# Performance work log

Measured on AMD Instinct MI355X. Metric: run time of the kernel, lower is better.

## Reference

```python
import jax, jax.numpy as jnp
import numpy as np

D_MODEL = 1024
NUM_HEADS = 16
HEAD_DIM = D_MODEL // NUM_HEADS


def setup_inputs() -> dict:
    key = jax.random.key(0)
    k1, k2, k3 = jax.random.split(key, 3)
    B, S = 2, 2048
    x = jax.random.normal(k1, (B, S, D_MODEL), dtype=jnp.float32)
    # causal mask: True = attend
    mask = jnp.tril(jnp.ones((S, S), dtype=bool))
    # bias-free Linear weights, y = x @ W.T; scaled init
    w_qkv = jax.random.normal(k2, (3 * D_MODEL, D_MODEL), dtype=jnp.float32) * (D_MODEL ** -0.5)
    w_o = jax.random.normal(k3, (D_MODEL, D_MODEL), dtype=jnp.float32) * (D_MODEL ** -0.5)
    return {"x": x, "mask": mask, "w_qkv": w_qkv, "w_o": w_o}


def reference(x, mask, w_qkv, w_o):
    B, S, _ = x.shape
    qkv = jnp.einsum('bsd,ed->bse', x, w_qkv)           # [B,S,3*d_model]
    q, k, v = jnp.split(qkv, 3, axis=-1)
    # [B,S,H*Dh] -> [B,H,S,Dh]
    def to_heads(t):
        return t.reshape(B, S, NUM_HEADS, HEAD_DIM).transpose(0, 2, 1, 3)
    q, k, v = to_heads(q), to_heads(k), to_heads(v)
    scale = jnp.asarray(HEAD_DIM, dtype=x.dtype) ** -0.5
    scores = jnp.einsum('bhnd,bhmd->bhnm', q, k) * scale  # [B,H,S,S]
    scores = jnp.where(mask, scores, jnp.asarray(-jnp.inf, dtype=scores.dtype))
    attn = jax.nn.softmax(scores, axis=-1)
    out = jnp.einsum('bhnm,bhmd->bhnd', attn, v)          # [B,H,S,Dh]
    out = out.transpose(0, 2, 1, 3).reshape(B, S, D_MODEL)
    return jnp.einsum('bsd,ed->bse', out, w_o)
```

## Files before the change

kernel.cpp:

```cpp
#include <hip/hip_runtime.h>

typedef __bf16 bf16x8 __attribute__((ext_vector_type(8)));
typedef float f32x4 __attribute__((ext_vector_type(4)));
typedef unsigned int u32;
typedef unsigned short u16;

#define DEV static __device__ __forceinline__

DEV u16 f2bf(float f){
  __bf16 h = (__bf16)f;
  u16 u; __builtin_memcpy(&u, &h, 2); return u;
}
DEV float bf2f(u16 u){
  u32 x = ((u32)u) << 16;
  float f; __builtin_memcpy(&f, &x, 4); return f;
}
DEV u32 pack2bf(float lo, float hi){
  return (u32)f2bf(lo) | ((u32)f2bf(hi) << 16);
}
DEV void gll16(void* lds, const void* g){
  __builtin_amdgcn_global_load_lds((const __attribute__((address_space(1))) void*)g,
                                   (__attribute__((address_space(3))) void*)lds, 16, 0, 0);
}

__global__ __launch_bounds__(256) void cast3_f32_bf16(
    const float* __restrict__ x, const float* __restrict__ wqkv,
    const float* __restrict__ wo, u16* __restrict__ xb,
    u16* __restrict__ wqkvb, u16* __restrict__ wob)
{
  const int NX = 1048576, NW = 786432, NO = 262144;
  int i = blockIdx.x * blockDim.x + threadIdx.x;
  int stride = gridDim.x * blockDim.x;
  for (; i < NX + NW + NO; i += stride){
    const float4* s; u16* d; int j;
    if (i < NX){ s = (const float4*)x; d = xb; j = i; }
    else if (i < NX + NW){ s = (const float4*)wqkv; d = wqkvb; j = i - NX; }
    else { s = (const float4*)wo; d = wob; j = i - NX - NW; }
    float4 v = s[j];
    ushort4 o;
    o.x = f2bf(v.x); o.y = f2bf(v.y); o.z = f2bf(v.z); o.w = f2bf(v.w);
    ((ushort4*)d)[j] = o;
  }
}

template<int BM, int BN, int MW>
__global__ __launch_bounds__(256, MW) void gemm_dbuf(
    const u16* __restrict__ A, const u16* __restrict__ B,
    u16* __restrict__ qbuf, u16* __restrict__ kbuf, u16* __restrict__ vbuf,
    float* __restrict__ fout, int mode)
{
  __shared__ __align__(16) u16 As[2][BM*32];
  __shared__ __align__(16) u16 Bs[2][BN*32];
  const int tid = threadIdx.x;
  const int ln  = tid & 63;
  const int w   = tid >> 6;
  const int wr = w >> 1, wc = w & 1;
  const int l15 = ln & 15, lg = ln >> 4;
  const int tM = blockIdx.y * BM, tN = blockIdx.x * BN;
  const int K = 1024;

  f32x4 acc[BM/32][BN/32] = {};

  const int grow = tid >> 2;
  const int gswz = ((tid & 3) ^ (grow & 3)) * 8;
  const u16* ap = A + (size_t)(tM + grow) * K + gswz;
  const u16* bp = B + (size_t)(tN + grow) * K + gswz;

  #define GSTAGE(buf_, k0_) do { \
    _Pragma("unroll") \
    for (int cc = 0; cc < BM/64; cc++) \
      gll16(&As[buf_][cc*2048 + w*512], ap + (size_t)cc*64*K + (k0_)); \
    _Pragma("unroll") \
    for (int cc = 0; cc < BN/64; cc++) \
      gll16(&Bs[buf_][cc*2048 + w*512], bp + (size_t)cc*64*K + (k0_)); \
  } while(0)

  #define WAITPREV() do { \
    if constexpr (BM/64 + BN/64 == 4) asm volatile("s_waitcnt vmcnt(4)" ::: "memory"); \
    else                              asm volatile("s_waitcnt vmcnt(3)" ::: "memory"); \
  } while(0)

  const int rg = (lg ^ (l15 & 3)) * 8;

  #define GCOMP(BUF) do { \
    bf16x8 af[BM/32], bfr[BN/32]; \
    _Pragma("unroll") \
    for (int m = 0; m < BM/32; m++) \
      af[m] = *(const bf16x8*)(&As[BUF][(wr*(BM/2) + m*16 + l15)*32 + rg]); \
    _Pragma("unroll") \
    for (int n = 0; n < BN/32; n++) \
      bfr[n] = *(const bf16x8*)(&Bs[BUF][(wc*(BN/2) + n*16 + l15)*32 + rg]); \
    _Pragma("unroll") \
    for (int m = 0; m < BM/32; m++) \
      _Pragma("unroll") \
      for (int n = 0; n < BN/32; n++) \
        acc[m][n] = __builtin_amdgcn_mfma_f32_16x16x32_bf16(af[m], bfr[n], acc[m][n], 0, 0, 0); \
  } while(0)

  GSTAGE(0, 0);
  #pragma unroll 1
  for (int k0 = 0; k0 < K; k0 += 64){
    if (k0 + 32 < K){
      GSTAGE(1, k0 + 32);
      WAITPREV();
    } else {
      asm volatile("s_waitcnt vmcnt(0)" ::: "memory");
    }
    __builtin_amdgcn_s_barrier();
    __builtin_amdgcn_sched_barrier(0);
    GCOMP(0);
    __builtin_amdgcn_s_barrier();
    if (k0 + 64 < K){
      GSTAGE(0, k0 + 64);
      WAITPREV();
    } else {
      asm volatile("s_waitcnt vmcnt(0)" ::: "memory");
    }
    __builtin_amdgcn_s_barrier();
    __builtin_amdgcn_sched_barrier(0);
    GCOMP(1);
    __builtin_amdgcn_s_barrier();
  }
  #undef GSTAGE
  #undef GCOMP
  #undef WAITPREV

  #pragma unroll
  for (int m = 0; m < BM/32; m++){
    #pragma unroll
    for (int n = 0; n < BN/32; n++){
      const int col = tN + wc*(BN/2) + n*16 + l15;
      const int rowb = tM + wr*(BM/2) + m*16 + lg*4;
      if (mode == 0){
        const int t = col >> 10, rem = col & 1023;
        const int h = rem >> 6, d = rem & 63;
        if (t == 2){
          const int b = rowb >> 11, s = rowb & 2047;
          ushort4 pk;
          pk.x = f2bf(acc[m][n][0]);
          pk.y = f2bf(acc[m][n][1]);
          pk.z = f2bf(acc[m][n][2]);
          pk.w = f2bf(acc[m][n][3]);
          *(ushort4*)(vbuf + ((size_t)(b*16 + h)*64 + d)*2048 + s) = pk;
        } else {
          #pragma unroll
          for (int r = 0; r < 4; r++){
            int row = rowb + r;
            int b = row >> 11, s = row & 2047;
            size_t idx = ((size_t)(b*16 + h)*2048 + s)*64 + d;
            if (t == 0) qbuf[idx] = f2bf(acc[m][n][r] * 0.125f);
            else        kbuf[idx] = f2bf(acc[m][n][r]);
          }
        }
      } else {
        #pragma unroll
        for (int r = 0; r < 4; r++)
          fout[(size_t)(rowb + r) * 1024 + col] = acc[m][n][r];
      }
    }
  }
}

__global__ __launch_bounds__(128) void attn_fwd(
    const u16* __restrict__ qb, const u16* __restrict__ kb,
    const u16* __restrict__ vt, u16* __restrict__ ob,
    u16* __restrict__ pO, float* __restrict__ pS)
{
  __shared__ __align__(16) u16 KVs[8192];
  const int tid = threadIdx.x;
  const int ln = tid & 63;
  const int w = tid >> 6;
  const int l15 = ln & 15, lg = ln >> 4;
  const float L2E = 1.4426950408889634f;

  const int B = blockIdx.x;
  const int xcd = B & 7;
  const int rest = B >> 3;
  const int bhl = rest & 3;
  const int j = rest >> 2;
  const int bh = xcd * 4 + bhl;
  int ti, t0, t1, split, c;
  if (j < 32){ ti = 32 + j; t0 = 0; t1 = 32; split = 1; c = 0; }
  else {
    int k = j - 32; int v = 32 - (k >> 1);
    if ((k & 1) == 0){ ti = v - 1;  t0 = 0;  t1 = ti + 1; split = 0; c = 0; }
    else             { ti = 31 + v; t0 = 32; t1 = ti + 1; split = 1; c = 1; }
  }
  const int nt = ti + 1;
  const int wq0 = ti * 32 + w * 16;
  const int b_out = bh >> 4, h_out = bh & 15;

  const int kg = (ln & 7) ^ (ln >> 3);
  const int vg = (ln & 3) ^ ((ln >> 3) & 3);
  const u16* kp0 = kb + ((size_t)bh*2048 + (ln >> 3))*64 + kg*8;
  const u16* vp0 = vt + ((size_t)bh*64  + (ln >> 2))*2048 + vg*8;

  #define STAGE(bf_, kv0_) do { \
    gll16(&KVs[(bf_)*2048 + (w*2 + 0)*512], kp0 + (size_t)((kv0_) + (w*2+0)*8)*64); \
    gll16(&KVs[(bf_)*2048 + (w*2 + 1)*512], kp0 + (size_t)((kv0_) + (w*2+1)*8)*64); \
    gll16(&KVs[4096 + (bf_)*2048 + (w*2 + 0)*512], vp0 + (size_t)((w*2+0)*16)*2048 + (kv0_)); \
    gll16(&KVs[4096 + (bf_)*2048 + (w*2 + 1)*512], vp0 + (size_t)((w*2+1)*16)*2048 + (kv0_)); \
  } while(0)

  bf16x8 qf[2];
  #pragma unroll
  for (int ks = 0; ks < 2; ks++)
    qf[ks] = *(const bf16x8*)(qb + ((size_t)bh*2048 + wq0 + l15)*64 + ks*32 + lg*8);

  f32x4 ot[4] = {};
  float m_run = -3e38f;
  float l_loc = 0.f;

  const int kb0 = l15*64 + (( lg      ^ (l15 & 7)) * 8);
  const int kb1 = l15*64 + (((4 + lg) ^ (l15 & 7)) * 8);
  const int vb  = l15*32 + (( lg ^ ((l15 >> 1) & 3)) * 8);
  const int s0l = l15 | ((lg & 1) << 5);
  const int s2l = s0l | 16;
  const bool hi = (lg >> 1) & 1;

  #define BODY(BUF) do { \
    const int kv0 = t * 32; \
    f32x4 st[2] = {}; \
    __builtin_amdgcn_s_setprio(1); \
    _Pragma("unroll") \
    for (int ks = 0; ks < 2; ks++){ \
      const int kb = ks ? kb1 : kb0; \
      bf16x8 kf[2]; \
      _Pragma("unroll") \
      for (int an = 0; an < 2; an++) \
        kf[an] = *(const bf16x8*)(&KVs[(BUF)*2048 + an*1024 + kb]); \
      _Pragma("unroll") \
      for (int an = 0; an < 2; an++) \
        st[an] = __builtin_amdgcn_mfma_f32_16x16x32_bf16(kf[an], qf[ks], st[an], 0, 0, 0); \
    } \
    __builtin_amdgcn_s_setprio(0); \
    if (t == nt - 1){ \
      _Pragma("unroll") \
      for (int an = 0; an < 2; an++) \
        _Pragma("unroll") \
        for (int rr = 0; rr < 4; rr++){ \
          int kv = kv0 + an*16 + lg*4 + rr; \
          int q  = wq0 + l15; \
          if (kv > q) st[an][rr] = -3e38f; \
        } \
    } \
    float mx0 = fmaxf(fmaxf(st[0][0], st[0][1]), fmaxf(st[0][2], st[0][3])); \
    float mx1 = fmaxf(fmaxf(st[1][0], st[1][1]), fmaxf(st[1][2], st[1][3])); \
    float lmax = fmaxf(mx0, mx1); \
    float m0 = m_run; \
    if (__any(lmax > m0 + 8.f)){ \
      float tmax = fmaxf(lmax, __shfl_xor(lmax, 16)); \
      tmax = fmaxf(tmax, __shfl_xor(tmax, 32)); \
      float mnew = fmaxf(m0, tmax); \
      float alpha = __builtin_amdgcn_exp2f((m0 - mnew) * L2E); \
      m_run = mnew; \
      l_loc *= alpha; \
      _Pragma("unroll") \
      for (int dm = 0; dm < 4; dm++){ \
        ot[dm][0] *= alpha; ot[dm][1] *= alpha; \
        ot[dm][2] *= alpha; ot[dm][3] *= alpha; \
      } \
      m0 = mnew; \
    } \
    u32 pk01[2], pk23[2]; \
    float psum[2]; \
    _Pragma("unroll") \
    for (int an = 0; an < 2; an++){ \
      float e0 = __builtin_amdgcn_exp2f((st[an][0] - m0) * L2E); \
      float e1 = __builtin_amdgcn_exp2f((st[an][1] - m0) * L2E); \
      float e2 = __builtin_amdgcn_exp2f((st[an][2] - m0) * L2E); \
      float e3 = __builtin_amdgcn_exp2f((st[an][3] - m0) * L2E); \
      psum[an] = (e0 + e1) + (e2 + e3); \
      pk01[an] = pack2bf(e0, e1); \
      pk23[an] = pack2bf(e2, e3); \
    } \
    l_loc += psum[0] + psum[1]; \
    bf16x8 vfr[4]; \
    _Pragma("unroll") \
    for (int dm = 0; dm < 4; dm++) \
      vfr[dm] = *(const bf16x8*)(&KVs[4096 + (BUF)*2048 + dm*512 + vb]); \
    u32 a0 = __shfl(pk01[0], s0l), b0 = __shfl(pk01[1], s0l); \
    u32 a1 = __shfl(pk23[0], s0l), b1 = __shfl(pk23[1], s0l); \
    u32 a2 = __shfl(pk01[0], s2l), b2 = __shfl(pk01[1], s2l); \
    u32 a3 = __shfl(pk23[0], s2l), b3 = __shfl(pk23[1], s2l); \
    union { u32 u[4]; bf16x8 v; } pf; \
    pf.u[0] = hi ? b0 : a0; \
    pf.u[1] = hi ? b1 : a1; \
    pf.u[2] = hi ? b2 : a2; \
    pf.u[3] = hi ? b3 : a3; \
    __builtin_amdgcn_s_setprio(1); \
    _Pragma("unroll") \
    for (int dm = 0; dm < 4; dm++) \
      ot[dm] = __builtin_amdgcn_mfma_f32_16x16x32_bf16(vfr[dm], pf.v, ot[dm], 0, 0, 0); \
    __builtin_amdgcn_s_setprio(0); \
  } while(0)

  STAGE(0, t0 * 32);
  int t = t0;
  #pragma unroll 1
  while (t < t1){
    if (t + 1 < t1){
      STAGE(1, (t + 1) * 32);
      asm volatile("s_waitcnt vmcnt(4)" ::: "memory");
    } else {
      asm volatile("s_waitcnt vmcnt(0)" ::: "memory");
    }
    __builtin_amdgcn_s_barrier();
    __builtin_amdgcn_sched_barrier(0);
    BODY(0);
    __builtin_amdgcn_s_barrier();
    t++;
    if (t >= t1) break;
    if (t + 1 < t1){
      STAGE(0, (t + 1) * 32);
      asm volatile("s_waitcnt vmcnt(4)" ::: "memory");
    } else {
      asm volatile("s_waitcnt vmcnt(0)" ::: "memory");
    }
    __builtin_amdgcn_s_barrier();
    __builtin_amdgcn_sched_barrier(0);
    BODY(1);
    __builtin_amdgcn_s_barrier();
    t++;
  }
  #undef STAGE
  #undef BODY

  float lsum = l_loc + __shfl_xor(l_loc, 16);
  lsum += __shfl_xor(lsum, 32);
  if (!split){
    float inv = 1.0f / lsum;
    int q = wq0 + l15;
    u16* obase = ob + (((size_t)b_out*2048 + q)*16 + h_out)*64 + lg*4;
    #pragma unroll
    for (int dm = 0; dm < 4; dm++){
      ushort4 pk;
      pk.x = f2bf(ot[dm][0] * inv);
      pk.y = f2bf(ot[dm][1] * inv);
      pk.z = f2bf(ot[dm][2] * inv);
      pk.w = f2bf(ot[dm][3] * inv);
      *(ushort4*)(obase + dm*16) = pk;
    }
  } else {
    const int sidx = (bh*32 + (ti - 32))*2 + c;
    const int qloc = w*16 + l15;
    u16* pbase = pO + (size_t)sidx*2048 + qloc*64 + lg*4;
    #pragma unroll
    for (int dm = 0; dm < 4; dm++){
      ushort4 pk;
      pk.x = f2bf(ot[dm][0]);
      pk.y = f2bf(ot[dm][1]);
      pk.z = f2bf(ot[dm][2]);
      pk.w = f2bf(ot[dm][3]);
      *(ushort4*)(pbase + dm*16) = pk;
    }
    if (lg == 0){
      pS[sidx*64 + qloc*2 + 0] = m_run;
      pS[sidx*64 + qloc*2 + 1] = lsum;
    }
  }
}

__global__ __launch_bounds__(128) void attn_combine(
    const u16* __restrict__ pO, const float* __restrict__ pS,
    u16* __restrict__ ob)
{
  const float L2E = 1.4426950408889634f;
  const int p = blockIdx.x;
  const int bh = p >> 5;
  const int ti = 32 + (p & 31);
  const int s0 = (bh*32 + (ti - 32))*2;
  const int tid = threadIdx.x;
  const int row = tid >> 2, seg = tid & 3;

  float m0 = pS[s0*64 + row*2],     l0 = pS[s0*64 + row*2 + 1];
  float m1 = pS[(s0+1)*64 + row*2], l1 = pS[(s0+1)*64 + row*2 + 1];
  float m = fmaxf(m0, m1);
  float f0 = __builtin_amdgcn_exp2f((m0 - m) * L2E);
  float f1 = __builtin_amdgcn_exp2f((m1 - m) * L2E);
  float inv = 1.0f / (l0*f0 + l1*f1);
  f0 *= inv; f1 *= inv;

  union { int4 v[2]; u16 u[16]; } o0, o1, od;
  const u16* p0 = pO + (size_t)s0*2048 + row*64 + seg*16;
  const u16* p1 = pO + (size_t)(s0+1)*2048 + row*64 + seg*16;
  o0.v[0] = ((const int4*)p0)[0]; o0.v[1] = ((const int4*)p0)[1];
  o1.v[0] = ((const int4*)p1)[0]; o1.v[1] = ((const int4*)p1)[1];
  #pragma unroll
  for (int i = 0; i < 16; i++)
    od.u[i] = f2bf(bf2f(o0.u[i])*f0 + bf2f(o1.u[i])*f1);

  const int b = bh >> 4, h = bh & 15;
  const int q = ti*32 + row;
  u16* dst = ob + (((size_t)b*2048 + q)*16 + h)*64 + seg*16;
  ((int4*)dst)[0] = od.v[0];
  ((int4*)dst)[1] = od.v[1];
}

extern "C" void kernel_launch(void* const* d_in, const int* in_sizes, int n_in,
                              void* d_out, int out_size, void* d_ws, size_t ws_size,
                              hipStream_t stream)
{
  (void)in_sizes; (void)n_in; (void)out_size; (void)ws_size;
  const float* x    = (const float*)d_in[0];
  const float* wqkv = (const float*)d_in[2];
  const float* wo   = (const float*)d_in[3];
  float* out = (float*)d_out;

  char* ws = (char*)d_ws;
  u16* xb    = (u16*)(ws);
  u16* wqkvb = (u16*)(ws + ((size_t)8  << 20));
  u16* wob   = (u16*)(ws + ((size_t)14 << 20));
  u16* qbuf  = (u16*)(ws + ((size_t)16 << 20));
  u16* kbuf  = (u16*)(ws + ((size_t)24 << 20));
  u16* vtbuf = (u16*)(ws + ((size_t)40 << 20));
  u16* obuf  = (u16*)(ws + ((size_t)48 << 20));
  u16*   pO = xb;
  float* pS = (float*)wqkvb;

  cast3_f32_bf16<<<2048, 256, 0, stream>>>(x, wqkv, wo, xb, wqkvb, wob);
  gemm_dbuf<128,128,3><<<dim3(24, 32), 256, 0, stream>>>(xb, wqkvb, qbuf, kbuf, vtbuf, nullptr, 0);
  attn_fwd<<<3072, 128, 0, stream>>>(qbuf, kbuf, vtbuf, obuf, pO, pS);
  attn_combine<<<1024, 128, 0, stream>>>(pO, pS, obuf);
  gemm_dbuf<64,128,6><<<dim3(8, 64), 256, 0, stream>>>(obuf, wob, nullptr, nullptr, nullptr, out, 1);
}
```

Measured before the change: 118.0 us.

## Load K/V fragments directly from global memory instead of LDS double buffering

Removes the shared-memory K/V staging (global_load_lds double buffer with barriers and waitcnt) from the attention kernel. Each wave now loads its K and V MFMA fragments straight from global memory into registers every tile. This drops LDS traffic and block-wide barriers, so waves can run independently. In exchange the two waves fetch the same K/V data redundantly, rely on cache hits, and lose the explicit prefetch overlap of the next tile.

```diff
diff --git a/kernel.cpp b/kernel.cpp
--- a/kernel.cpp
+++ b/kernel.cpp
@@ -166,7 +166,6 @@
     const u16* __restrict__ vt, u16* __restrict__ ob,
     u16* __restrict__ pO, float* __restrict__ pS)
 {
-  __shared__ __align__(16) u16 KVs[8192];
   const int tid = threadIdx.x;
   const int ln = tid & 63;
   const int w = tid >> 6;
@@ -190,17 +189,8 @@
   const int wq0 = ti * 32 + w * 16;
   const int b_out = bh >> 4, h_out = bh & 15;
 
-  const int kg = (ln & 7) ^ (ln >> 3);
-  const int vg = (ln & 3) ^ ((ln >> 3) & 3);
-  const u16* kp0 = kb + ((size_t)bh*2048 + (ln >> 3))*64 + kg*8;
-  const u16* vp0 = vt + ((size_t)bh*64  + (ln >> 2))*2048 + vg*8;
-
-  #define STAGE(bf_, kv0_) do { \
-    gll16(&KVs[(bf_)*2048 + (w*2 + 0)*512], kp0 + (size_t)((kv0_) + (w*2+0)*8)*64); \
-    gll16(&KVs[(bf_)*2048 + (w*2 + 1)*512], kp0 + (size_t)((kv0_) + (w*2+1)*8)*64); \
-    gll16(&KVs[4096 + (bf_)*2048 + (w*2 + 0)*512], vp0 + (size_t)((w*2+0)*16)*2048 + (kv0_)); \
-    gll16(&KVs[4096 + (bf_)*2048 + (w*2 + 1)*512], vp0 + (size_t)((w*2+1)*16)*2048 + (kv0_)); \
-  } while(0)
+  const u16* kfp = kb + ((size_t)bh*2048 + l15)*64 + lg*8;
+  const u16* vfp = vt + ((size_t)bh*64 + l15)*2048 + lg*8;
 
   bf16x8 qf[2];
   #pragma unroll
@@ -211,120 +201,93 @@
   float m_run = -3e38f;
   float l_loc = 0.f;
 
-  const int kb0 = l15*64 + (( lg      ^ (l15 & 7)) * 8);
-  const int kb1 = l15*64 + (((4 + lg) ^ (l15 & 7)) * 8);
-  const int vb  = l15*32 + (( lg ^ ((l15 >> 1) & 3)) * 8);
   const int s0l = l15 | ((lg & 1) << 5);
   const int s2l = s0l | 16;
   const bool hi = (lg >> 1) & 1;
 
-  #define BODY(BUF) do { \
-    const int kv0 = t * 32; \
-    f32x4 st[2] = {}; \
-    __builtin_amdgcn_s_setprio(1); \
-    _Pragma("unroll") \
-    for (int ks = 0; ks < 2; ks++){ \
-      const int kb = ks ? kb1 : kb0; \
-      bf16x8 kf[2]; \
-      _Pragma("unroll") \
-      for (int an = 0; an < 2; an++) \
-        kf[an] = *(const bf16x8*)(&KVs[(BUF)*2048 + an*1024 + kb]); \
-      _Pragma("unroll") \
-      for (int an = 0; an < 2; an++) \
-        st[an] = __builtin_amdgcn_mfma_f32_16x16x32_bf16(kf[an], qf[ks], st[an], 0, 0, 0); \
-    } \
-    __builtin_amdgcn_s_setprio(0); \
-    if (t == nt - 1){ \
-      _Pragma("unroll") \
-      for (int an = 0; an < 2; an++) \
-        _Pragma("unroll") \
-        for (int rr = 0; rr < 4; rr++){ \
-          int kv = kv0 + an*16 + lg*4 + rr; \
-          int q  = wq0 + l15; \
-          if (kv > q) st[an][rr] = -3e38f; \
-        } \
-    } \
-    float mx0 = fmaxf(fmaxf(st[0][0], st[0][1]), fmaxf(st[0][2], st[0][3])); \
-    float mx1 = fmaxf(fmaxf(st[1][0], st[1][1]), fmaxf(st[1][2], st[1][3])); \
-    float lmax = fmaxf(mx0, mx1); \
-    float m0 = m_run; \
-    if (__any(lmax > m0 + 8.f)){ \
-      float tmax = fmaxf(lmax, __shfl_xor(lmax, 16)); \
-      tmax = fmaxf(tmax, __shfl_xor(tmax, 32)); \
-      float mnew = fmaxf(m0, tmax); \
-      float alpha = __builtin_amdgcn_exp2f((m0 - mnew) * L2E); \
-      m_run = mnew; \
-      l_loc *= alpha; \
-      _Pragma("unroll") \
-      for (int dm = 0; dm < 4; dm++){ \
-        ot[dm][0] *= alpha; ot[dm][1] *= alpha; \
-        ot[dm][2] *= alpha; ot[dm][3] *= alpha; \
-      } \
-      m0 = mnew; \
-    } \
-    u32 pk01[2], pk23[2]; \
-    float psum[2]; \
-    _Pragma("unroll") \
-    for (int an = 0; an < 2; an++){ \
-      float e0 = __builtin_amdgcn_exp2f((st[an][0] - m0) * L2E); \
-      float e1 = __builtin_amdgcn_exp2f((st[an][1] - m0) * L2E); \
-      float e2 = __builtin_amdgcn_exp2f((st[an][2] - m0) * L2E); \
-      float e3 = __builtin_amdgcn_exp2f((st[an][3] - m0) * L2E); \
-      psum[an] = (e0 + e1) + (e2 + e3); \
-      pk01[an] = pack2bf(e0, e1); \
-      pk23[an] = pack2bf(e2, e3); \
-    } \
-    l_loc += psum[0] + psum[1]; \
-    bf16x8 vfr[4]; \
-    _Pragma("unroll") \
-    for (int dm = 0; dm < 4; dm++) \
-      vfr[dm] = *(const bf16x8*)(&KVs[4096 + (BUF)*2048 + dm*512 + vb]); \
-    u32 a0 = __shfl(pk01[0], s0l), b0 = __shfl(pk01[1], s0l); \
-    u32 a1 = __shfl(pk23[0], s0l), b1 = __shfl(pk23[1], s0l); \
-    u32 a2 = __shfl(pk01[0], s2l), b2 = __shfl(pk01[1], s2l); \
-    u32 a3 = __shfl(pk23[0], s2l), b3 = __shfl(pk23[1], s2l); \
-    union { u32 u[4]; bf16x8 v; } pf; \
-    pf.u[0] = hi ? b0 : a0; \
-    pf.u[1] = hi ? b1 : a1; \
-    pf.u[2] = hi ? b2 : a2; \
-    pf.u[3] = hi ? b3 : a3; \
-    __builtin_amdgcn_s_setprio(1); \
-    _Pragma("unroll") \
-    for (int dm = 0; dm < 4; dm++) \
-      ot[dm] = __builtin_amdgcn_mfma_f32_16x16x32_bf16(vfr[dm], pf.v, ot[dm], 0, 0, 0); \
-    __builtin_amdgcn_s_setprio(0); \
-  } while(0)
-
-  STAGE(0, t0 * 32);
-  int t = t0;
   #pragma unroll 1
-  while (t < t1){
-    if (t + 1 < t1){
-      STAGE(1, (t + 1) * 32);
-      asm volatile("s_waitcnt vmcnt(4)" ::: "memory");
-    } else {
-      asm volatile("s_waitcnt vmcnt(0)" ::: "memory");
-    }
-    __builtin_amdgcn_s_barrier();
-    __builtin_amdgcn_sched_barrier(0);
-    BODY(0);
-    __builtin_amdgcn_s_barrier();
-    t++;
-    if (t >= t1) break;
-    if (t + 1 < t1){
-      STAGE(0, (t + 1) * 32);
-      asm volatile("s_waitcnt vmcnt(4)" ::: "memory");
-    } else {
-      asm volatile("s_waitcnt vmcnt(0)" ::: "memory");
-    }
-    __builtin_amdgcn_s_barrier();
-    __builtin_amdgcn_sched_barrier(0);
-    BODY(1);
-    __builtin_amdgcn_s_barrier();
-    t++;
-  }
-  #undef STAGE
-  #undef BODY
+  for (int t = t0; t < t1; t++){
+    const int kv0 = t * 32;
+    bf16x8 kf[2][2];
+    #pragma unroll
+    for (int ks = 0; ks < 2; ks++)
+      #pragma unroll
+      for (int an = 0; an < 2; an++)
+        kf[ks][an] = *(const bf16x8*)(kfp + (size_t)(kv0 + an*16)*64 + ks*32);
+    bf16x8 vfr[4];
+    #pragma unroll
+    for (int dm = 0; dm < 4; dm++)
+      vfr[dm] = *(const bf16x8*)(vfp + (size_t)dm*32768 + kv0);
+
+    f32x4 st[2] = {};
+    __builtin_amdgcn_s_setprio(1);
+    #pragma unroll
+    for (int ks = 0; ks < 2; ks++)
+      #pragma unroll
+      for (int an = 0; an < 2; an++)
+        st[an] = __builtin_amdgcn_mfma_f32_16x16x32_bf16(kf[ks][an], qf[ks], st[an], 0, 0, 0);
+    __builtin_amdgcn_s_setprio(0);
+
+    if (t == nt - 1){
+      #pragma unroll
+      for (int an = 0; an < 2; an++)
+        #pragma unroll
+        for (int rr = 0; rr < 4; rr++){
+          int kv = kv0 + an*16 + lg*4 + rr;
+          int q  = wq0 + l15;
+          if (kv > q) st[an][rr] = -3e38f;
+        }
+    }
+
+    float mx0 = fmaxf(fmaxf(st[0][0], st[0][1]), fmaxf(st[0][2], st[0][3]));
+    float mx1 = fmaxf(fmaxf(st[1][0], st[1][1]), fmaxf(st[1][2], st[1][3]));
+    float lmax = fmaxf(mx0, mx1);
+    float m0 = m_run;
+    if (__any(lmax > m0 + 8.f)){
+      float tmax = fmaxf(lmax, __shfl_xor(lmax, 16));
+      tmax = fmaxf(tmax, __shfl_xor(tmax, 32));
+      float mnew = fmaxf(m0, tmax);
+      float alpha = __builtin_amdgcn_exp2f((m0 - mnew) * L2E);
+      m_run = mnew;
+      l_loc *= alpha;
+      #pragma unroll
+      for (int dm = 0; dm < 4; dm++){
+        ot[dm][0] *= alpha; ot[dm][1] *= alpha;
+        ot[dm][2] *= alpha; ot[dm][3] *= alpha;
+      }
+      m0 = mnew;
+    }
+
+    u32 pk01[2], pk23[2];
+    float psum[2];
+    #pragma unroll
+    for (int an = 0; an < 2; an++){
+      float e0 = __builtin_amdgcn_exp2f((st[an][0] - m0) * L2E);
+      float e1 = __builtin_amdgcn_exp2f((st[an][1] - m0) * L2E);
+      float e2 = __builtin_amdgcn_exp2f((st[an][2] - m0) * L2E);
+      float e3 = __builtin_amdgcn_exp2f((st[an][3] - m0) * L2E);
+      psum[an] = (e0 + e1) + (e2 + e3);
+      pk01[an] = pack2bf(e0, e1);
+      pk23[an] = pack2bf(e2, e3);
+    }
+    l_loc += psum[0] + psum[1];
+
+    u32 a0 = __shfl(pk01[0], s0l), b0 = __shfl(pk01[1], s0l);
+    u32 a1 = __shfl(pk23[0], s0l), b1 = __shfl(pk23[1], s0l);
+    u32 a2 = __shfl(pk01[0], s2l), b2 = __shfl(pk01[1], s2l);
+    u32 a3 = __shfl(pk23[0], s2l), b3 = __shfl(pk23[1], s2l);
+    union { u32 u[4]; bf16x8 v; } pf;
+    pf.u[0] = hi ? b0 : a0;
+    pf.u[1] = hi ? b1 : a1;
+    pf.u[2] = hi ? b2 : a2;
+    pf.u[3] = hi ? b3 : a3;
+
+    __builtin_amdgcn_s_setprio(1);
+    #pragma unroll
+    for (int dm = 0; dm < 4; dm++)
+      ot[dm] = __builtin_amdgcn_mfma_f32_16x16x32_bf16(vfr[dm], pf.v, ot[dm], 0, 0, 0);
+    __builtin_amdgcn_s_setprio(0);
+  }
 
   float lsum = l_loc + __shfl_xor(l_loc, 16);
   lsum += __shfl_xor(lsum, 32);
```

New measurement: 200.4 us. 69.8% more time.

## Load K/V fragments directly from global into registers, dropping LDS staging

Applied to the files above, without the earlier changes.

The attention kernel stops staging K and V tiles through shared memory with global_load_lds and barriers. Each wave now loads its MFMA operand fragments straight from global memory into registers, double-buffered across two register sets. This removes the LDS round trip and the workgroup barriers. In exchange each of the two waves fetches the same K/V data redundantly, the accesses are less coalesced (V rows strided by 2048), and register pressure rises.

```diff
diff --git a/kernel.cpp b/kernel.cpp
--- a/kernel.cpp
+++ b/kernel.cpp
@@ -166,7 +166,6 @@
     const u16* __restrict__ vt, u16* __restrict__ ob,
     u16* __restrict__ pO, float* __restrict__ pS)
 {
-  __shared__ __align__(16) u16 KVs[8192];
   const int tid = threadIdx.x;
   const int ln = tid & 63;
   const int w = tid >> 6;
@@ -190,17 +189,8 @@
   const int wq0 = ti * 32 + w * 16;
   const int b_out = bh >> 4, h_out = bh & 15;
 
-  const int kg = (ln & 7) ^ (ln >> 3);
-  const int vg = (ln & 3) ^ ((ln >> 3) & 3);
-  const u16* kp0 = kb + ((size_t)bh*2048 + (ln >> 3))*64 + kg*8;
-  const u16* vp0 = vt + ((size_t)bh*64  + (ln >> 2))*2048 + vg*8;
-
-  #define STAGE(bf_, kv0_) do { \
-    gll16(&KVs[(bf_)*2048 + (w*2 + 0)*512], kp0 + (size_t)((kv0_) + (w*2+0)*8)*64); \
-    gll16(&KVs[(bf_)*2048 + (w*2 + 1)*512], kp0 + (size_t)((kv0_) + (w*2+1)*8)*64); \
-    gll16(&KVs[4096 + (bf_)*2048 + (w*2 + 0)*512], vp0 + (size_t)((w*2+0)*16)*2048 + (kv0_)); \
-    gll16(&KVs[4096 + (bf_)*2048 + (w*2 + 1)*512], vp0 + (size_t)((w*2+1)*16)*2048 + (kv0_)); \
-  } while(0)
+  const u16* kfp = kb + ((size_t)bh*2048 + l15)*64 + lg*8;
+  const u16* vfp = vt + ((size_t)bh*64 + l15)*2048 + lg*8;
 
   bf16x8 qf[2];
   #pragma unroll
@@ -211,28 +201,31 @@
   float m_run = -3e38f;
   float l_loc = 0.f;
 
-  const int kb0 = l15*64 + (( lg      ^ (l15 & 7)) * 8);
-  const int kb1 = l15*64 + (((4 + lg) ^ (l15 & 7)) * 8);
-  const int vb  = l15*32 + (( lg ^ ((l15 >> 1) & 3)) * 8);
   const int s0l = l15 | ((lg & 1) << 5);
   const int s2l = s0l | 16;
   const bool hi = (lg >> 1) & 1;
 
-  #define BODY(BUF) do { \
+  #define LOADT(KF, VF, tt) do { \
+    const size_t kvo = (size_t)(tt) * 32; \
+    _Pragma("unroll") \
+    for (int ks = 0; ks < 2; ks++) \
+      _Pragma("unroll") \
+      for (int an = 0; an < 2; an++) \
+        KF[ks][an] = *(const bf16x8*)(kfp + (kvo + an*16)*64 + ks*32); \
+    _Pragma("unroll") \
+    for (int dm = 0; dm < 4; dm++) \
+      VF[dm] = *(const bf16x8*)(vfp + (size_t)dm*32768 + kvo); \
+  } while(0)
+
+  #define BODYR(KF, VF) do { \
     const int kv0 = t * 32; \
     f32x4 st[2] = {}; \
     __builtin_amdgcn_s_setprio(1); \
     _Pragma("unroll") \
-    for (int ks = 0; ks < 2; ks++){ \
-      const int kb = ks ? kb1 : kb0; \
-      bf16x8 kf[2]; \
+    for (int ks = 0; ks < 2; ks++) \
       _Pragma("unroll") \
       for (int an = 0; an < 2; an++) \
-        kf[an] = *(const bf16x8*)(&KVs[(BUF)*2048 + an*1024 + kb]); \
-      _Pragma("unroll") \
-      for (int an = 0; an < 2; an++) \
-        st[an] = __builtin_amdgcn_mfma_f32_16x16x32_bf16(kf[an], qf[ks], st[an], 0, 0, 0); \
-    } \
+        st[an] = __builtin_amdgcn_mfma_f32_16x16x32_bf16(KF[ks][an], qf[ks], st[an], 0, 0, 0); \
     __builtin_amdgcn_s_setprio(0); \
     if (t == nt - 1){ \
       _Pragma("unroll") \
@@ -275,10 +268,6 @@
       pk23[an] = pack2bf(e2, e3); \
     } \
     l_loc += psum[0] + psum[1]; \
-    bf16x8 vfr[4]; \
-    _Pragma("unroll") \
-    for (int dm = 0; dm < 4; dm++) \
-      vfr[dm] = *(const bf16x8*)(&KVs[4096 + (BUF)*2048 + dm*512 + vb]); \
     u32 a0 = __shfl(pk01[0], s0l), b0 = __shfl(pk01[1], s0l); \
     u32 a1 = __shfl(pk23[0], s0l), b1 = __shfl(pk23[1], s0l); \
     u32 a2 = __shfl(pk01[0], s2l), b2 = __shfl(pk01[1], s2l); \
@@ -291,40 +280,25 @@
     __builtin_amdgcn_s_setprio(1); \
     _Pragma("unroll") \
     for (int dm = 0; dm < 4; dm++) \
-      ot[dm] = __builtin_amdgcn_mfma_f32_16x16x32_bf16(vfr[dm], pf.v, ot[dm], 0, 0, 0); \
+      ot[dm] = __builtin_amdgcn_mfma_f32_16x16x32_bf16(VF[dm], pf.v, ot[dm], 0, 0, 0); \
     __builtin_amdgcn_s_setprio(0); \
   } while(0)
 
-  STAGE(0, t0 * 32);
+  bf16x8 kfA[2][2], vfA[4], kfB[2][2], vfB[4];
+  LOADT(kfA, vfA, t0);
   int t = t0;
   #pragma unroll 1
   while (t < t1){
-    if (t + 1 < t1){
-      STAGE(1, (t + 1) * 32);
-      asm volatile("s_waitcnt vmcnt(4)" ::: "memory");
-    } else {
-      asm volatile("s_waitcnt vmcnt(0)" ::: "memory");
-    }
-    __builtin_amdgcn_s_barrier();
-    __builtin_amdgcn_sched_barrier(0);
-    BODY(0);
-    __builtin_amdgcn_s_barrier();
+    if (t + 1 < t1) LOADT(kfB, vfB, t + 1);
+    BODYR(kfA, vfA);
     t++;
     if (t >= t1) break;
-    if (t + 1 < t1){
-      STAGE(0, (t + 1) * 32);
-      asm volatile("s_waitcnt vmcnt(4)" ::: "memory");
-    } else {
-      asm volatile("s_waitcnt vmcnt(0)" ::: "memory");
-    }
-    __builtin_amdgcn_s_barrier();
-    __builtin_amdgcn_sched_barrier(0);
-    BODY(1);
-    __builtin_amdgcn_s_barrier();
+    if (t + 1 < t1) LOADT(kfA, vfA, t + 1);
+    BODYR(kfB, vfB);
     t++;
   }
-  #undef STAGE
-  #undef BODY
+  #undef LOADT
+  #undef BODYR
 
   float lsum = l_loc + __shfl_xor(l_loc, 16);
   lsum += __shfl_xor(lsum, 32);
```

Result: slower. 190.5 us (+61.4%).
